# Optimization experiments

Hardware: AMD Instinct MI355X
Metric: run time of the kernel (lower is better)

Reference implementation:

```python
import jax, jax.numpy as jnp
import numpy as np

IN_CH = 1024   # backbone channels
N_T = 81       # n_targets (COCO classes + bg)
K = 7          # PSROI grid size
H = 100        # feature map height
WID = 100      # feature map width
R = 1024       # number of regions
S = 2          # bilinear sampling points per bin edge (PSROIAlign-style average)


def setup_inputs() -> dict:
    key = jax.random.key(0)
    k1, k2, k3 = jax.random.split(key, 3)
    x = jax.random.normal(k1, (IN_CH, H, WID), dtype=jnp.float32)
    # regions: fractional (i, j, h, w) = (center_y, center_x, height, width) in [0,1]
    regions = jax.random.uniform(k2, (R, 4), dtype=jnp.float32)
    conv_w = jax.random.normal(k3, (N_T * K * K, IN_CH), dtype=jnp.float32) * 0.02
    conv_b = jnp.zeros((N_T * K * K,), dtype=jnp.float32)
    return {"x": x, "regions": regions, "conv_w": conv_w, "conv_b": conv_b}


def _bilinear_pool(map_thw, ys, xs):
    """Average of bilinear samples of one bin's score map.

    map_thw: (T, H, W) score map for this (u, v) bin's channel group.
    ys: (R, S) sample row coords.  xs: (R, S) sample col coords.
    Returns (R, T): per-region average-pooled bin value.
    """
    Hm, Wm = map_thw.shape[1], map_thw.shape[2]
    ys = jnp.clip(ys, 0.0, Hm - 1)
    xs = jnp.clip(xs, 0.0, Wm - 1)
    y0 = jnp.floor(ys)
    x0 = jnp.floor(xs)
    y0i = y0.astype(jnp.int32)
    x0i = x0.astype(jnp.int32)
    y1i = jnp.minimum(y0i + 1, Hm - 1)
    x1i = jnp.minimum(x0i + 1, Wm - 1)
    wy1 = ys - y0
    wy0 = 1.0 - wy1
    wx1 = xs - x0
    wx0 = 1.0 - wx1

    def g(yi, xi):  # gather (T, R, S, S)
        return map_thw[:, yi[:, :, None], xi[:, None, :]]

    v = (g(y0i, x0i) * (wy0[:, :, None] * wx0[:, None, :])
         + g(y0i, x1i) * (wy0[:, :, None] * wx1[:, None, :])
         + g(y1i, x0i) * (wy1[:, :, None] * wx0[:, None, :])
         + g(y1i, x1i) * (wy1[:, :, None] * wx1[:, None, :]))
    return v.mean((2, 3)).T  # (R, T)


def reference(x, regions, conv_w, conv_b):
    # 1x1 conv score map: (n_targets*k^2, H, W)
    sm = jnp.einsum('oc,chw->ohw', conv_w, x) + conv_b[:, None, None]
    sm = sm.reshape(N_T, K, K, H, WID)  # (T, ky, kx, H, W) position-sensitive groups

    # region geometry (fractional center/size -> absolute feature-map coords)
    top = (regions[:, 0] - regions[:, 2] * 0.5) * H     # (R,)
    left = (regions[:, 1] - regions[:, 3] * 0.5) * WID  # (R,)
    bh = regions[:, 2] * H / K                          # bin height
    bw = regions[:, 3] * WID / K                        # bin width

    off = (jnp.arange(S, dtype=jnp.float32) + 0.5) / S  # (S,) sample offsets in bin
    bins = jnp.arange(K, dtype=jnp.float32)             # (K,)
    ys = top[:, None, None] + (bins[None, :, None] + off[None, None, :]) * bh[:, None, None]   # (R,K,S)
    xs = left[:, None, None] + (bins[None, :, None] + off[None, None, :]) * bw[:, None, None]  # (R,K,S)

    # vmap over the k x k position-sensitive bins; bin (u,v) reads channel group (:,u,v)
    inner = jax.vmap(_bilinear_pool, in_axes=(1, None, 1))  # over kx: sm axis, xs axis
    outer = jax.vmap(inner, in_axes=(1, 1, None))           # over ky: sm axis, ys axis
    pooled = outer(sm, ys, xs)  # (K, K, R, T)

    # pooled.mean(-1).mean(-1) over the k x k grid
    scores = pooled.mean((0, 1))  # (R, T)
    return scores
```

## Files before the change

### kernel.cpp

```cpp
#include <hip/hip_runtime.h>
#include <cstddef>

#define IN_CH 1024
#define NT    81
#define KGRID 7
#define NBINS 49
#define HH    100
#define WW    100
#define NPIX  (HH*WW)
#define NREG  1024
#define COLB  82
#define NCOL  (NBINS*COLB)
#define NPADW 4096
#define SROW  NCOL
#define PXB   ((NPIX + 31) / 32)
#define PXG   (PXB * (IN_CH / 128))
#define PREPG (PXG + NPADW)

typedef unsigned short ushortT;
typedef short bf16x8 __attribute__((ext_vector_type(8)));
typedef float f32x4  __attribute__((ext_vector_type(4)));

static __device__ __forceinline__ unsigned short f2bf(float f) {
    unsigned int u = __builtin_bit_cast(unsigned int, f);
    return (unsigned short)((u + 0x7fffu + ((u >> 16) & 1u)) >> 16);
}
static __device__ __forceinline__ float bf_lo(unsigned int v) {
    return __builtin_bit_cast(float, v << 16);
}
static __device__ __forceinline__ float bf_hi(unsigned int v) {
    return __builtin_bit_cast(float, v & 0xffff0000u);
}

static __device__ __forceinline__ void gld_lds16(const ushortT* g, ushortT* l) {
    __builtin_amdgcn_global_load_lds(
        (__attribute__((address_space(1))) void*)(unsigned long long)(uintptr_t)g,
        (__attribute__((address_space(3))) void*)(unsigned int)(unsigned long long)(uintptr_t)l,
        16, 0, 0);
}

__global__ __launch_bounds__(256) void prep_fused(const float* __restrict__ x,
                                                  ushortT* __restrict__ xbT,
                                                  const float* __restrict__ conv_w,
                                                  ushortT* __restrict__ Wr) {
    __shared__ float tile[128][33];
    const int tid = threadIdx.x;
    const int bid = blockIdx.x;
    if (bid < PXG) {
        const int p0 = (bid % PXB) * 32;
        const int c0 = (bid / PXB) * 128;
        const int pl = tid & 31;
        const int cg = tid >> 5;
        const int p = p0 + pl;
#pragma unroll
        for (int it = 0; it < 16; ++it) {
            const int c = it * 8 + cg;
            tile[c][pl] = (p < NPIX) ? x[(size_t)(c0 + c) * NPIX + p] : 0.0f;
        }
        __syncthreads();
#pragma unroll
        for (int pass = 0; pass < 2; ++pass) {
            const int pix = pass * 16 + (tid >> 4);
            const int cb  = (tid & 15) * 8;
            if (p0 + pix < NPIX) {
                uint4 pk;
                pk.x = (unsigned int)f2bf(tile[cb + 0][pix]) | ((unsigned int)f2bf(tile[cb + 1][pix]) << 16);
                pk.y = (unsigned int)f2bf(tile[cb + 2][pix]) | ((unsigned int)f2bf(tile[cb + 3][pix]) << 16);
                pk.z = (unsigned int)f2bf(tile[cb + 4][pix]) | ((unsigned int)f2bf(tile[cb + 5][pix]) << 16);
                pk.w = (unsigned int)f2bf(tile[cb + 6][pix]) | ((unsigned int)f2bf(tile[cb + 7][pix]) << 16);
                *(uint4*)(xbT + (size_t)(p0 + pix) * IN_CH + c0 + cb) = pk;
            }
        }
    } else {
        const int row = bid - PXG;
        const int bin = row / COLB;
        const int t   = row - bin * COLB;
        const int c   = tid * 4;
        uint2 pk; pk.x = 0; pk.y = 0;
        if (bin < NBINS && t < NT) {
            const float4 v = *(const float4*)(conv_w + ((size_t)(t * NBINS + bin)) * IN_CH + c);
            pk.x = (unsigned int)f2bf(v.x) | ((unsigned int)f2bf(v.y) << 16);
            pk.y = (unsigned int)f2bf(v.z) | ((unsigned int)f2bf(v.w) << 16);
        }
        *(uint2*)(Wr + (size_t)row * IN_CH + c) = pk;
    }
}

__global__ __launch_bounds__(256) void gemm_sm(const ushortT* __restrict__ xbT,
                                               const ushortT* __restrict__ Wr,
                                               ushortT* __restrict__ sm) {
    __shared__ ushortT a_lds[128 * 32];
    __shared__ ushortT b_lds[128 * 32];
    const int tid  = threadIdx.x;
    const int lane = tid & 63;
    const int w    = tid >> 6;
    const int wm   = w & 1;
    const int wn   = w >> 1;
    const int n0   = blockIdx.x * 128;
    const int p0   = blockIdx.y * 128;

    const int srow0 = w * 32 + (lane >> 2);
    const int scol  = (lane & 3) * 8;
    int ap0 = p0 + srow0;      if (ap0 > NPIX - 1) ap0 = NPIX - 1;
    int ap1 = p0 + srow0 + 16; if (ap1 > NPIX - 1) ap1 = NPIX - 1;
    const ushortT* ag0 = xbT + (size_t)ap0 * IN_CH + scol;
    const ushortT* ag1 = xbT + (size_t)ap1 * IN_CH + scol;
    const ushortT* bg0 = Wr + (size_t)(n0 + srow0) * IN_CH + scol;
    const ushortT* bg1 = Wr + (size_t)(n0 + srow0 + 16) * IN_CH + scol;
    ushortT* al0 = a_lds + (w * 32) * 32;
    ushortT* al1 = a_lds + (w * 32 + 16) * 32;
    ushortT* bl0 = b_lds + (w * 32) * 32;
    ushortT* bl1 = b_lds + (w * 32 + 16) * 32;

    const int m_lane = lane & 15;
    const int k0     = (lane >> 4) * 8;

    f32x4 acc[4][4];
#pragma unroll
    for (int mt = 0; mt < 4; ++mt)
#pragma unroll
        for (int nt = 0; nt < 4; ++nt) acc[mt][nt] = (f32x4){0.f, 0.f, 0.f, 0.f};

    for (int kc = 0; kc < IN_CH / 32; ++kc) {
        __syncthreads();
        gld_lds16(ag0, al0);
        gld_lds16(ag1, al1);
        gld_lds16(bg0, bl0);
        gld_lds16(bg1, bl1);
        ag0 += 32; ag1 += 32; bg0 += 32; bg1 += 32;
        __syncthreads();

        bf16x8 af[4], bf[4];
#pragma unroll
        for (int mt = 0; mt < 4; ++mt)
            af[mt] = *(const bf16x8*)(a_lds + (wm * 64 + mt * 16 + m_lane) * 32 + k0);
#pragma unroll
        for (int nt = 0; nt < 4; ++nt)
            bf[nt] = *(const bf16x8*)(b_lds + (wn * 64 + nt * 16 + m_lane) * 32 + k0);
#pragma unroll
        for (int mt = 0; mt < 4; ++mt)
#pragma unroll
            for (int nt = 0; nt < 4; ++nt)
                acc[mt][nt] = __builtin_amdgcn_mfma_f32_16x16x32_bf16(af[mt], bf[nt], acc[mt][nt], 0, 0, 0);
    }

    const int prow_base = p0 + wm * 64 + (lane >> 4) * 4;
    const int ncol_base = n0 + wn * 64 + m_lane;
#pragma unroll
    for (int mt = 0; mt < 4; ++mt) {
#pragma unroll
        for (int rg = 0; rg < 4; ++rg) {
            const int p = prow_base + mt * 16 + rg;
            if (p < NPIX) {
                ushortT* rowp = sm + (size_t)p * SROW;
#pragma unroll
                for (int nt = 0; nt < 4; ++nt) {
                    const int n = ncol_base + nt * 16;
                    if (n < NCOL) rowp[n] = f2bf(acc[mt][nt][rg]);
                }
            }
        }
    }
}

__global__ __launch_bounds__(256) void pool_kernel(const ushortT* __restrict__ sm,
                                                   const float* __restrict__ regions,
                                                   const float* __restrict__ conv_b,
                                                   float* __restrict__ out) {
    __shared__ int   rowo[28]; __shared__ float roww[28];
    __shared__ int   coli[28]; __shared__ float colw[28];
    __shared__ int   pofs[784];
    __shared__ float pw[784];
    __shared__ float part[6][COLB];
    const int tid = threadIdx.x;
    const int r = blockIdx.x;

    if (tid < 28) {
        const float4 reg = *(const float4*)(regions + (size_t)r * 4);
        const float top = (reg.x - reg.z * 0.5f) * (float)HH;
        const float bh  = reg.z * ((float)HH / (float)KGRID);
        const int u = tid >> 2, i = tid & 3;
        const int s = i >> 1, hi = i & 1;
        float y = top + ((float)u + ((float)s + 0.5f) * 0.5f) * bh;
        y = fminf(fmaxf(y, 0.0f), (float)(HH - 1));
        const float y0f = floorf(y);
        const int y0 = (int)y0f;
        const float wy1 = y - y0f;
        rowo[tid] = (hi ? min(y0 + 1, HH - 1) : y0) * WW;
        roww[tid] = hi ? wy1 : (1.0f - wy1);
    } else if (tid >= 32 && tid < 60) {
        const float4 reg = *(const float4*)(regions + (size_t)r * 4);
        const float left = (reg.y - reg.w * 0.5f) * (float)WW;
        const float bw   = reg.w * ((float)WW / (float)KGRID);
        const int idx = tid - 32;
        const int v = idx >> 2, j = idx & 3;
        const int s = j >> 1, hi = j & 1;
        float xx = left + ((float)v + ((float)s + 0.5f) * 0.5f) * bw;
        xx = fminf(fmaxf(xx, 0.0f), (float)(WW - 1));
        const float x0f = floorf(xx);
        const int x0 = (int)x0f;
        const float wx1 = xx - x0f;
        coli[idx] = hi ? min(x0 + 1, WW - 1) : x0;
        colw[idx] = hi ? wx1 : (1.0f - wx1);
    }
    __syncthreads();
    for (int tt = tid; tt < 784; tt += 256) {
        const int bin = tt >> 4, tap = tt & 15;
        const int u = bin / KGRID, v = bin - u * KGRID;
        const int i = tap >> 2, j = tap & 3;
        const int pix = rowo[u * 4 + i] + coli[v * 4 + j];
        pofs[tt] = pix * SROW + bin * COLB;
        pw[tt]   = roww[u * 4 + i] * colw[v * 4 + j] * (1.0f / 196.0f);
    }
    __syncthreads();

    const int tg    = tid / 41;
    const int cslot = tid - tg * 41;
    if (tg < 6) {
        float a0 = 0.f, a1 = 0.f;
        const int l2 = cslot * 2;
        for (int lt = tg; lt < 784; lt += 6) {
            const unsigned int v = *(const unsigned int*)(sm + pofs[lt] + l2);
            const float wt = pw[lt];
            a0 += wt * bf_lo(v);
            a1 += wt * bf_hi(v);
        }
        part[tg][l2] = a0; part[tg][l2 + 1] = a1;
    }
    __syncthreads();
    if (tid < NT) {
        float v = part[0][tid] + part[1][tid] + part[2][tid]
                + part[3][tid] + part[4][tid] + part[5][tid];
        float bsum = 0.f;
        for (int bin = 0; bin < NBINS; ++bin) bsum += conv_b[tid * NBINS + bin];
        out[(size_t)r * NT + tid] = v + bsum * (1.0f / (float)NBINS);
    }
}

__global__ __launch_bounds__(256) void xpose_kernel(const float* __restrict__ x,
                                                    float* __restrict__ xt) {
    __shared__ float tile[32][33];
    const int p0 = blockIdx.x * 32;
    const int c0 = blockIdx.y * 32;
    const int tx = threadIdx.x;
    const int ty = threadIdx.y;
#pragma unroll
    for (int k = 0; k < 32; k += 8) {
        const int p = p0 + tx;
        if (p < NPIX) tile[ty + k][tx] = x[(size_t)(c0 + ty + k) * NPIX + p];
    }
    __syncthreads();
#pragma unroll
    for (int k = 0; k < 32; k += 8) {
        const int p = p0 + ty + k;
        if (p < NPIX) xt[(size_t)p * IN_CH + (c0 + tx)] = tile[tx][ty + k];
    }
}

template <bool XPOSED>
__global__ __launch_bounds__(256) void psroi_kernel(
    const float* __restrict__ xsrc, const float* __restrict__ regions,
    const float* __restrict__ conv_w, const float* __restrict__ conv_b,
    float* __restrict__ out) {
    __shared__ float w_lds[32 * 96];
    __shared__ float g_lds[32 * 64];
    __shared__ int   rowoff[64][4];
    __shared__ float rowwf[64][4];
    __shared__ int   colidx[64][4];
    __shared__ float colwf[64][4];
    const int tid = threadIdx.x;
    const int bin = blockIdx.x >> 4;
    const int rg  = blockIdx.x & 15;
    const int u = bin / KGRID, v = bin % KGRID;
    const int r0 = rg * 64;
    if (tid < 64) {
        const float4 reg = *(const float4*)(regions + (size_t)(r0 + tid) * 4);
        const float top  = (reg.x - reg.z * 0.5f) * (float)HH;
        const float left = (reg.y - reg.w * 0.5f) * (float)WW;
        const float bh = reg.z * ((float)HH / (float)KGRID);
        const float bw = reg.w * ((float)WW / (float)KGRID);
        const float scale = 1.0f / 196.0f;
#pragma unroll
        for (int s = 0; s < 2; s++) {
            const float off = (s + 0.5f) * 0.5f;
            float yy = top + ((float)u + off) * bh;
            yy = fminf(fmaxf(yy, 0.0f), (float)(HH - 1));
            const float y0f = floorf(yy);
            const int y0 = (int)y0f;
            const float wy1 = yy - y0f;
            rowoff[tid][2 * s] = y0 * WW;
            rowoff[tid][2 * s + 1] = min(y0 + 1, HH - 1) * WW;
            rowwf[tid][2 * s] = (1.0f - wy1) * scale;
            rowwf[tid][2 * s + 1] = wy1 * scale;
            float xx = left + ((float)v + off) * bw;
            xx = fminf(fmaxf(xx, 0.0f), (float)(WW - 1));
            const float x0f = floorf(xx);
            const int x0 = (int)x0f;
            const float wx1 = xx - x0f;
            colidx[tid][2 * s] = x0;
            colidx[tid][2 * s + 1] = min(x0 + 1, WW - 1);
            colwf[tid][2 * s] = 1.0f - wx1;
            colwf[tid][2 * s + 1] = wx1;
        }
    }
    const int ri = tid & 15, tq = tid >> 4, rb = tid >> 2, cq = tid & 3;
    float acc[4][6];
#pragma unroll
    for (int m = 0; m < 4; m++)
#pragma unroll
        for (int k = 0; k < 6; k++) acc[m][k] = 0.0f;
    for (int chunk = 0; chunk < IN_CH / 32; chunk++) {
        const int c0 = chunk * 32;
        __syncthreads();
#pragma unroll
        for (int it = 0; it < 12; it++) {
            const int idx = it * 256 + tid;
            const int t = idx >> 5, c = idx & 31;
            float val = 0.0f;
            if (t < NT) val = conv_w[(size_t)(t * NBINS + bin) * IN_CH + c0 + c];
            w_lds[c * 96 + t] = val;
        }
        const int cbase = c0 + cq * 8;
        float g8[8];
#pragma unroll
        for (int cc = 0; cc < 8; cc++) g8[cc] = 0.0f;
#pragma unroll
        for (int i = 0; i < 4; i++) {
            const int ro = rowoff[rb][i];
            const float wy = rowwf[rb][i];
#pragma unroll
            for (int j = 0; j < 4; j++) {
                const int pix = ro + colidx[rb][j];
                const float wv = wy * colwf[rb][j];
                if (XPOSED) {
                    const float4* p = (const float4*)(xsrc + (size_t)pix * IN_CH + cbase);
                    const float4 a = p[0]; const float4 b = p[1];
                    g8[0] += wv * a.x; g8[1] += wv * a.y; g8[2] += wv * a.z; g8[3] += wv * a.w;
                    g8[4] += wv * b.x; g8[5] += wv * b.y; g8[6] += wv * b.z; g8[7] += wv * b.w;
                } else {
#pragma unroll
                    for (int cc = 0; cc < 8; cc++)
                        g8[cc] += wv * xsrc[(size_t)(cbase + cc) * NPIX + pix];
                }
            }
        }
#pragma unroll
        for (int cc = 0; cc < 8; cc++) g_lds[(cq * 8 + cc) * 64 + rb] = g8[cc];
        __syncthreads();
#pragma unroll 4
        for (int c = 0; c < 32; c++) {
            float wv[6];
#pragma unroll
            for (int k = 0; k < 6; k++) wv[k] = w_lds[c * 96 + tq * 6 + k];
            const float4 gq = *(const float4*)&g_lds[c * 64 + ri * 4];
            const float gm[4] = {gq.x, gq.y, gq.z, gq.w};
#pragma unroll
            for (int m = 0; m < 4; m++)
#pragma unroll
                for (int k = 0; k < 6; k++) acc[m][k] += gm[m] * wv[k];
        }
    }
    const float invK2 = 1.0f / 49.0f;
#pragma unroll
    for (int k = 0; k < 6; k++) {
        const int t = tq * 6 + k;
        if (t < NT) {
            const float bterm = conv_b[t * NBINS + bin] * invK2;
#pragma unroll
            for (int m = 0; m < 4; m++) {
                const int rr = r0 + ri * 4 + m;
                atomicAdd(&out[(size_t)rr * NT + t], acc[m][k] + bterm);
            }
        }
    }
}

extern "C" void kernel_launch(void* const* d_in, const int* in_sizes, int n_in,
                              void* d_out, int out_size, void* d_ws, size_t ws_size,
                              hipStream_t stream) {
    const float* x       = (const float*)d_in[0];
    const float* regions = (const float*)d_in[1];
    const float* conv_w  = (const float*)d_in[2];
    const float* conv_b  = (const float*)d_in[3];
    float* out = (float*)d_out;

    const size_t sz_xbT = (size_t)NPIX * IN_CH * 2;
    const size_t sz_Wr  = (size_t)NPADW * IN_CH * 2;
    const size_t sz_sm  = (size_t)NPIX * SROW * 2;
    const size_t need   = sz_xbT + sz_Wr + sz_sm;

    if (ws_size >= need) {
        ushortT* xbT = (ushortT*)d_ws;
        ushortT* Wr  = (ushortT*)((char*)d_ws + sz_xbT);
        ushortT* sm  = (ushortT*)((char*)d_ws + sz_xbT + sz_Wr);
        prep_fused<<<dim3(PREPG), 256, 0, stream>>>(x, xbT, conv_w, Wr);
        gemm_sm<<<dim3(NPADW / 128, (NPIX + 127) / 128), 256, 0, stream>>>(xbT, Wr, sm);
        pool_kernel<<<dim3(NREG), 256, 0, stream>>>(sm, regions, conv_b, out);
    } else {
        hipMemsetAsync(out, 0, (size_t)out_size * sizeof(float), stream);
        const size_t xt_bytes = (size_t)NPIX * IN_CH * sizeof(float);
        const dim3 mainGrid(NBINS * 16);
        if (ws_size >= xt_bytes) {
            float* xt = (float*)d_ws;
            xpose_kernel<<<dim3((NPIX + 31) / 32, IN_CH / 32), dim3(32, 8), 0, stream>>>(x, xt);
            psroi_kernel<true><<<mainGrid, 256, 0, stream>>>(xt, regions, conv_w, conv_b, out);
        } else {
            psroi_kernel<false><<<mainGrid, 256, 0, stream>>>(x, regions, conv_w, conv_b, out);
        }
    }
}
```

Measured before the change: 261.9 us.

## Split PSROI pooling across 8 blocks per region with batched 8-byte gathers

The pool kernel now launches a 2D grid (region × 8 groups), and each block handles 98 of the 784 bilinear taps. Each block then reduces over 12 streams of 9 taps, with each thread loading 4 bf16 channels per gather and issuing all 9 loads before accumulating. Partial sums are combined with atomicAdd into a zeroed output, and the bias is added only by group 0. This raises parallelism and memory-level parallelism for the gather-bound pooling, at the cost of an extra memset, atomics, and slightly over-read padding in the workspace.

```diff
diff --git a/kernel.cpp b/kernel.cpp
--- a/kernel.cpp
+++ b/kernel.cpp
@@ -13,6 +13,7 @@
 #define NCOL  (NBINS*COLB)
 #define NPADW 4096
 #define SROW  NCOL
+#define NG    8
 #define PXB   ((NPIX + 31) / 32)
 #define PXG   (PXB * (IN_CH / 128))
 #define PREPG (PXG + NPADW)
@@ -169,11 +170,12 @@
                                                    float* __restrict__ out) {
     __shared__ int   rowo[28]; __shared__ float roww[28];
     __shared__ int   coli[28]; __shared__ float colw[28];
-    __shared__ int   pofs[784];
-    __shared__ float pw[784];
-    __shared__ float part[6][COLB];
+    __shared__ int   pofs[108];
+    __shared__ float pw[108];
+    __shared__ float part[12][84];
     const int tid = threadIdx.x;
     const int r = blockIdx.x;
+    const int g = blockIdx.y;
 
     if (tid < 28) {
         const float4 reg = *(const float4*)(regions + (size_t)r * 4);
@@ -204,36 +206,53 @@
         colw[idx] = hi ? wx1 : (1.0f - wx1);
     }
     __syncthreads();
-    for (int tt = tid; tt < 784; tt += 256) {
-        const int bin = tt >> 4, tap = tt & 15;
-        const int u = bin / KGRID, v = bin - u * KGRID;
-        const int i = tap >> 2, j = tap & 3;
-        const int pix = rowo[u * 4 + i] + coli[v * 4 + j];
-        pofs[tt] = pix * SROW + bin * COLB;
-        pw[tt]   = roww[u * 4 + i] * colw[v * 4 + j] * (1.0f / 196.0f);
+    if (tid < 108) {
+        if (tid < 98) {
+            const int tt = g * 98 + tid;
+            const int bin = tt >> 4, tap = tt & 15;
+            const int u = bin / KGRID, v = bin - u * KGRID;
+            const int i = tap >> 2, j = tap & 3;
+            const int pix = rowo[u * 4 + i] + coli[v * 4 + j];
+            pofs[tid] = pix * SROW + bin * COLB;
+            pw[tid]   = roww[u * 4 + i] * colw[v * 4 + j] * (1.0f / 196.0f);
+        } else {
+            pofs[tid] = 0;
+            pw[tid]   = 0.0f;
+        }
     }
     __syncthreads();
 
-    const int tg    = tid / 41;
-    const int cslot = tid - tg * 41;
-    if (tg < 6) {
-        float a0 = 0.f, a1 = 0.f;
-        const int l2 = cslot * 2;
-        for (int lt = tg; lt < 784; lt += 6) {
-            const unsigned int v = *(const unsigned int*)(sm + pofs[lt] + l2);
-            const float wt = pw[lt];
-            a0 += wt * bf_lo(v);
-            a1 += wt * bf_hi(v);
-        }
-        part[tg][l2] = a0; part[tg][l2 + 1] = a1;
+    const int lane = tid & 63, w = tid >> 6;
+    const int sub  = lane / 21;
+    const int cidx = lane - sub * 21;
+    if (sub < 3) {
+        const int str = w * 3 + sub;
+        const int l2  = cidx * 4;
+        uint2 v[9];
+#pragma unroll
+        for (int it = 0; it < 9; ++it)
+            v[it] = *(const uint2*)(sm + pofs[str * 9 + it] + l2);
+        float a0 = 0.f, a1 = 0.f, a2 = 0.f, a3 = 0.f;
+#pragma unroll
+        for (int it = 0; it < 9; ++it) {
+            const float wt = pw[str * 9 + it];
+            a0 += wt * bf_lo(v[it].x); a1 += wt * bf_hi(v[it].x);
+            a2 += wt * bf_lo(v[it].y); a3 += wt * bf_hi(v[it].y);
+        }
+        float4 p4; p4.x = a0; p4.y = a1; p4.z = a2; p4.w = a3;
+        *(float4*)&part[str][l2] = p4;
     }
     __syncthreads();
     if (tid < NT) {
-        float v = part[0][tid] + part[1][tid] + part[2][tid]
-                + part[3][tid] + part[4][tid] + part[5][tid];
-        float bsum = 0.f;
-        for (int bin = 0; bin < NBINS; ++bin) bsum += conv_b[tid * NBINS + bin];
-        out[(size_t)r * NT + tid] = v + bsum * (1.0f / (float)NBINS);
+        float v = 0.f;
+#pragma unroll
+        for (int s = 0; s < 12; ++s) v += part[s][tid];
+        if (g == 0) {
+            float bsum = 0.f;
+            for (int bin = 0; bin < NBINS; ++bin) bsum += conv_b[tid * NBINS + bin];
+            v += bsum * (1.0f / (float)NBINS);
+        }
+        atomicAdd(out + (size_t)r * NT + tid, v);
     }
 }
 
@@ -386,16 +405,17 @@
 
     const size_t sz_xbT = (size_t)NPIX * IN_CH * 2;
     const size_t sz_Wr  = (size_t)NPADW * IN_CH * 2;
-    const size_t sz_sm  = (size_t)NPIX * SROW * 2;
+    const size_t sz_sm  = (size_t)NPIX * SROW * 2 + 256;
     const size_t need   = sz_xbT + sz_Wr + sz_sm;
 
     if (ws_size >= need) {
         ushortT* xbT = (ushortT*)d_ws;
         ushortT* Wr  = (ushortT*)((char*)d_ws + sz_xbT);
         ushortT* sm  = (ushortT*)((char*)d_ws + sz_xbT + sz_Wr);
+        hipMemsetAsync(out, 0, (size_t)out_size * sizeof(float), stream);
         prep_fused<<<dim3(PREPG), 256, 0, stream>>>(x, xbT, conv_w, Wr);
         gemm_sm<<<dim3(NPADW / 128, (NPIX + 127) / 128), 256, 0, stream>>>(xbT, Wr, sm);
-        pool_kernel<<<dim3(NREG), 256, 0, stream>>>(sm, regions, conv_b, out);
+        pool_kernel<<<dim3(NREG, NG), 256, 0, stream>>>(sm, regions, conv_b, out);
     } else {
         hipMemsetAsync(out, 0, (size_t)out_size * sizeof(float), stream);
         const size_t xt_bytes = (size_t)NPIX * IN_CH * sizeof(float);
```

Result: faster. 233.4 us (-10.9%).
